# Performance work log

Hardware: AMD Instinct MI355X
Metric: run time of the kernel (lower is better)

## Reference

```python
import jax, jax.numpy as jnp
import numpy as np

N, E = 50000, 800000          # nodes, edges (before self loops)
IN_DIM, HID = 128, 96
HEADS, LAYERS = 2, 2
C = HID // HEADS              # per-head channels = 48
NEG_SLOPE = 0.2               # PyG GATv2 leaky_relu slope
EPS = 1e-5                    # LayerNorm eps


def setup_inputs() -> dict:
    key = jax.random.key(0)
    ks = jax.random.split(key, 8)
    s = 0.05
    x = jax.random.normal(ks[0], (N, IN_DIM), jnp.float32)
    edge_index = jax.random.randint(ks[1], (2, E), 0, N, jnp.int32)
    Wp = jax.random.normal(ks[2], (IN_DIM, HID), jnp.float32) * s
    bp = jnp.zeros((HID,), jnp.float32)
    g0 = jnp.ones((HID,), jnp.float32)
    b0 = jnp.zeros((HID,), jnp.float32)
    Wl = jax.random.normal(ks[3], (LAYERS, HID, HID), jnp.float32) * s
    Wr = jax.random.normal(ks[4], (LAYERS, HID, HID), jnp.float32) * s
    att = jax.random.normal(ks[5], (LAYERS, HEADS, C), jnp.float32) * s
    gs = jnp.ones((LAYERS, HID), jnp.float32)
    bs = jnp.zeros((LAYERS, HID), jnp.float32)
    return dict(x=x, edge_index=edge_index, Wp=Wp, bp=bp, g0=g0, b0=b0,
                Wl=Wl, Wr=Wr, att=att, gs=gs, bs=bs)


def layer_norm(h, g, b):
    mu = jnp.mean(h, axis=-1, keepdims=True)
    var = jnp.mean(jnp.square(h - mu), axis=-1, keepdims=True)
    return (h - mu) * jax.lax.rsqrt(var + EPS) * g + b


def gatv2_layer(h, src, dst, Wl, Wr, att):
    # GATv2Conv, bias=False, concat=True, eval-mode (no attention dropout)
    xl = (h @ Wl).reshape(N, HEADS, C)   # source transform
    xr = (h @ Wr).reshape(N, HEADS, C)   # target transform
    e = jax.nn.leaky_relu(xl[src] + xr[dst], NEG_SLOPE)   # [Et,H,C]
    score = jnp.einsum('ehc,hc->eh', e, att)              # [Et,H]
    # segment softmax over edges grouped by target node
    m = jax.ops.segment_max(score, dst, num_segments=N)   # [N,H]
    p = jnp.exp(score - m[dst])
    denom = jax.ops.segment_sum(p, dst, num_segments=N)
    alpha = p / denom[dst]                                # [Et,H]
    out = jax.ops.segment_sum(alpha[:, :, None] * xl[src], dst, num_segments=N)
    return out.reshape(N, HID)


def reference(x, edge_index, Wp, bp, g0, b0, Wl, Wr, att, gs, bs):
    # add_self_loops=True: every node gets a self edge, so every segment is non-empty
    loops = jnp.arange(N, dtype=edge_index.dtype)
    src = jnp.concatenate([edge_index[0], loops])
    dst = jnp.concatenate([edge_index[1], loops])
    # input proj -> LayerNorm -> ReLU (dropout = identity in eval)
    h = jax.nn.relu(layer_norm(x @ Wp + bp, g0, b0))
    for i in range(LAYERS):
        hn = gatv2_layer(h, src, dst, Wl[i], Wr[i], att[i])
        hn = jax.nn.elu(layer_norm(hn, gs[i], bs[i]))
        h = h + hn   # shapes always match (HID -> HID), so residual always taken
    return h
```

## Files before the change

### kernel.cpp

```cpp
#include <hip/hip_runtime.h>
#include <hip/hip_bf16.h>

#define N_NODES 50000
#define E_EDGES 800000
#define ET (E_EDGES + N_NODES)
#define IN_DIM 128
#define HID 96
#define HEADS 2
#define CPH 48
#define NEG_SLOPE 0.2f
#define LN_EPS 1e-5f
#define CHUNK 24
#define LROW 50
#define PBASE (CHUNK * LROW)
#define WTILE (PBASE + 2 * CHUNK)
#define FBLK 2048
#define WPTOT (IN_DIM * HID)
#define WCTOT (HID * 2 * HID)

typedef __hip_bfloat16 bf16;
typedef short bf16x8 __attribute__((ext_vector_type(8)));
typedef float f32x4 __attribute__((ext_vector_type(4)));
typedef _Float16 h16;
typedef h16 h16x2 __attribute__((ext_vector_type(2)));
typedef h16 h16x8 __attribute__((ext_vector_type(8)));
typedef unsigned short ushort_t;

#if __has_builtin(__builtin_amdgcn_fdot2)
#define HAS_FDOT2 1
#else
#define HAS_FDOT2 0
#endif

#define CVTPK(dst, a, b) asm("v_cvt_pk_bf16_f32 %0, %1, %2" : "=v"(dst) : "v"(a), "v"(b))

__device__ __forceinline__ unsigned short f2bf(float f) {
    union { float f; unsigned int i; } u; u.f = f;
    unsigned int r = u.i + 0x7FFFu + ((u.i >> 16) & 1u);
    return (unsigned short)(r >> 16);
}

template<int CTRL>
__device__ __forceinline__ float dpp_add(float v) {
    int m = __builtin_amdgcn_update_dpp(0, __builtin_bit_cast(int, v), CTRL, 0xf, 0xf, false);
    return v + __builtin_bit_cast(float, m);
}
__device__ __forceinline__ float half_sum(float v) {
    v = dpp_add<0x111>(v); v = dpp_add<0x112>(v); v = dpp_add<0x114>(v);
    v = dpp_add<0x118>(v); v = dpp_add<0x142>(v);
    return v;
}
__device__ __forceinline__ float wave_sum(float v) {
    v = half_sum(v); v = dpp_add<0x143>(v);
    return v;
}
__device__ __forceinline__ float rlane(float v, int lane) {
    return __builtin_bit_cast(float, __builtin_amdgcn_readlane(__builtin_bit_cast(int, v), lane));
}

__global__ void k_hist(const int* __restrict__ ei, int* __restrict__ deg) {
    int e = blockIdx.x * blockDim.x + threadIdx.x;
    if (e >= ET) return;
    int dst = (e < E_EDGES) ? ei[E_EDGES + e] : (e - E_EDGES);
    atomicAdd(&deg[dst], 1);
}

__global__ __launch_bounds__(1024) void k_scan(const int* __restrict__ deg,
                                               int* __restrict__ rowstart,
                                               int* __restrict__ cursor) {
    __shared__ int wsum[16];
    __shared__ int s_carry;
    int t = threadIdx.x, lane = t & 63, w = t >> 6;
    if (t == 0) s_carry = 0;
    __syncthreads();
    for (int base = 0; base < N_NODES; base += 4096) {
        int i0 = base + t * 4;
        int4 d = {0, 0, 0, 0};
        if (i0 + 3 < N_NODES) d = *(const int4*)(deg + i0);
        else {
            if (i0 + 0 < N_NODES) d.x = deg[i0 + 0];
            if (i0 + 1 < N_NODES) d.y = deg[i0 + 1];
            if (i0 + 2 < N_NODES) d.z = deg[i0 + 2];
            if (i0 + 3 < N_NODES) d.w = deg[i0 + 3];
        }
        int e1 = d.x, e2 = d.x + d.y, e3 = d.x + d.y + d.z;
        int tot = e3 + d.w;
        int sv = tot;
        for (int o = 1; o < 64; o <<= 1) { int u = __shfl_up(sv, o, 64); if (lane >= o) sv += u; }
        if (lane == 63) wsum[w] = sv;
        __syncthreads();
        if (w == 0) {
            int val = (lane < 16) ? wsum[lane] : 0;
            int s2 = val;
            for (int o = 1; o < 64; o <<= 1) { int u = __shfl_up(s2, o, 64); if (lane >= o) s2 += u; }
            if (lane < 16) wsum[lane] = s2 - val;
        }
        __syncthreads();
        int excl = s_carry + wsum[w] + (sv - tot);
        if (i0 + 3 < N_NODES) {
            int4 r = {excl, excl + e1, excl + e2, excl + e3};
            *(int4*)(rowstart + i0) = r;
            *(int4*)(cursor + i0) = r;
        } else {
            if (i0 + 0 < N_NODES) { rowstart[i0 + 0] = excl;      cursor[i0 + 0] = excl; }
            if (i0 + 1 < N_NODES) { rowstart[i0 + 1] = excl + e1; cursor[i0 + 1] = excl + e1; }
            if (i0 + 2 < N_NODES) { rowstart[i0 + 2] = excl + e2; cursor[i0 + 2] = excl + e2; }
            if (i0 + 3 < N_NODES) { rowstart[i0 + 3] = excl + e3; cursor[i0 + 3] = excl + e3; }
        }
        __syncthreads();
        if (t == 1023) s_carry += wsum[15] + sv;
        __syncthreads();
    }
    if (t == 0) rowstart[N_NODES] = ET;
}

__global__ void k_scatter(const int* __restrict__ ei, int* __restrict__ cursor,
                          int* __restrict__ csr_src) {
    int e = blockIdx.x * blockDim.x + threadIdx.x;
    if (e >= ET) return;
    int src, dst;
    if (e < E_EDGES) { src = ei[e]; dst = ei[E_EDGES + e]; }
    else             { src = dst = e - E_EDGES; }
    int pos = atomicAdd(&cursor[dst], 1);
    csr_src[pos] = src;
}

__global__ void k_wprep_all(const float* __restrict__ Wp,
                            const float* __restrict__ Wl,
                            const float* __restrict__ Wr,
                            unsigned short* __restrict__ wp_frag,
                            unsigned short* __restrict__ wc_frag,
                            int* __restrict__ deg) {
    int idx = blockIdx.x * blockDim.x + threadIdx.x;
    if (idx < N_NODES) deg[idx] = 0;
    if (idx < WPTOT) {
        int j = idx & 7, lane = (idx >> 3) & 63;
        int nt = (idx >> 9) % 6, ks = (idx >> 9) / 6;
        int k = ks * 32 + ((lane >> 4) << 3) + j;
        int col = nt * 16 + (lane & 15);
        wp_frag[idx] = f2bf(Wp[k * HID + col]);
    } else if (idx < WPTOT + 2 * WCTOT) {
        int L = (idx - WPTOT) / WCTOT;
        int id = (idx - WPTOT) % WCTOT;
        int j = id & 7, lane = (id >> 3) & 63;
        int nt = (id >> 9) % 12, ks = (id >> 9) / 12;
        int k = ks * 32 + ((lane >> 4) << 3) + j;
        int col = nt * 16 + (lane & 15);
        const float* W0 = Wl + (size_t)L * HID * HID;
        const float* W1 = Wr + (size_t)L * HID * HID;
        float v = (col < HID) ? W0[k * HID + col] : W1[k * HID + col - HID];
        wc_frag[(size_t)L * WCTOT + id] = f2bf(v);
    }
}

template<int K, int NT, bool PROJ>
__global__ __launch_bounds__(256) void k_gemm(const float* __restrict__ A,
                                              const ushort_t* __restrict__ Abf,
                                              const unsigned short* __restrict__ Bfrag,
                                              const float* __restrict__ bp,
                                              const float* __restrict__ g0,
                                              const float* __restrict__ b0,
                                              float* __restrict__ hout,
                                              ushort_t* __restrict__ hbout,
                                              h16* __restrict__ xl,
                                              h16* __restrict__ xr) {
    constexpr int KS = K / 32;
    constexpr int NF = KS * NT;
    __shared__ unsigned short Blds[NF * 512];
    int t = threadIdx.x, l = t & 63, w = t >> 6;
    #pragma unroll
    for (int i = 0; i < NF / 4; i++)
        ((float4*)Blds)[i * 256 + t] = ((const float4*)Bfrag)[i * 256 + t];
    __syncthreads();

    int row0 = blockIdx.x * 64 + w * 16;
    int arow = row0 + (l & 15);
    if (arow > N_NODES - 1) arow = N_NODES - 1;
    int kb = (l >> 4) * 8;
    bf16x8 a[KS];
    if constexpr (PROJ) {
        const float* ap = A + (long)arow * K + kb;
        #pragma unroll
        for (int ks = 0; ks < KS; ks++) {
            float4 f0 = *(const float4*)(ap + ks * 32);
            float4 f1 = *(const float4*)(ap + ks * 32 + 4);
            union { unsigned int u[4]; bf16x8 v; } cv;
            CVTPK(cv.u[0], f0.x, f0.y); CVTPK(cv.u[1], f0.z, f0.w);
            CVTPK(cv.u[2], f1.x, f1.y); CVTPK(cv.u[3], f1.z, f1.w);
            a[ks] = cv.v;
        }
    } else {
        const ushort_t* ap = Abf + (long)arow * K + kb;
        #pragma unroll
        for (int ks = 0; ks < KS; ks++)
            a[ks] = *(const bf16x8*)(ap + ks * 32);
    }
    f32x4 acc[NT];
    #pragma unroll
    for (int nt = 0; nt < NT; nt++) acc[nt] = (f32x4){0.f, 0.f, 0.f, 0.f};
    #pragma unroll
    for (int nt = 0; nt < NT; nt++) {
        #pragma unroll
        for (int ks = 0; ks < KS; ks++) {
            bf16x8 b = *(const bf16x8*)(Blds + (((ks * NT + nt) * 64 + l) << 3));
            acc[nt] = __builtin_amdgcn_mfma_f32_16x16x32_bf16(a[ks], b, acc[nt], 0, 0, 0);
        }
    }
    int rg = l >> 4, cl = l & 15;
    if constexpr (PROJ) {
        float bpv[NT], g0v[NT], b0v[NT];
        #pragma unroll
        for (int nt = 0; nt < NT; nt++) {
            int col = nt * 16 + cl;
            bpv[nt] = bp[col]; g0v[nt] = g0[col]; b0v[nt] = b0[col];
        }
        #pragma unroll
        for (int r = 0; r < 4; r++) {
            float s = 0.f, sq = 0.f;
            #pragma unroll
            for (int nt = 0; nt < NT; nt++) {
                float v = acc[nt][r] + bpv[nt];
                acc[nt][r] = v; s += v; sq += v * v;
            }
            #pragma unroll
            for (int o = 1; o <= 8; o <<= 1) { s += __shfl_xor(s, o, 64); sq += __shfl_xor(sq, o, 64); }
            float mu = s / (float)HID;
            float var = sq / (float)HID - mu * mu;
            float rstd = rsqrtf(var + LN_EPS);
            int row = row0 + rg * 4 + r;
            if (row < N_NODES) {
                #pragma unroll
                for (int nt = 0; nt < NT; nt++) {
                    int col = nt * 16 + cl;
                    float y = fmaxf((acc[nt][r] - mu) * rstd * g0v[nt] + b0v[nt], 0.f);
                    hout[(long)row * HID + col] = y;
                    hbout[(long)row * HID + col] = f2bf(y);
                }
            }
        }
    } else {
        #pragma unroll
        for (int r = 0; r < 4; r++) {
            int row = row0 + rg * 4 + r;
            if (row < N_NODES) {
                #pragma unroll
                for (int nt = 0; nt < NT; nt++) {
                    int col = nt * 16 + cl;
                    h16 v = (h16)acc[nt][r];
                    if (col < HID) xl[(long)row * HID + col] = v;
                    else           xr[(long)row * HID + col - HID] = v;
                }
            }
        }
    }
}

__global__ __launch_bounds__(256) void k_node_fused(const int* __restrict__ rowstart,
                                                    const int* __restrict__ csr_src,
                                                    const h16* __restrict__ xl,
                                                    const h16* __restrict__ xr,
                                                    const float* __restrict__ att,
                                                    const float* __restrict__ gs,
                                                    const float* __restrict__ bs,
                                                    float* __restrict__ h,
                                                    ushort_t* __restrict__ hb,
                                                    float* __restrict__ out,
                                                    int write_out) {
    __shared__ float lds[4 * WTILE];
    int t = threadIdx.x, lane = t & 63, w = t >> 6;
    float* slds = lds + w * WTILE;
    float* pbuf = slds + PBASE;
    int j = lane & 31, hh = lane >> 5;
    bool jok = (j < CHUNK);
    int l = lane;
    int lc = (l < 48) ? l : 47;
    bool hi = (lc >= 24);
    bool act = (l < 48);

    const float* ar = att + hh * CPH;
    h16x8 attv[6];
    #pragma unroll
    for (int v = 0; v < 6; v++) {
        float4 t0 = *(const float4*)(ar + v * 8);
        float4 t1 = *(const float4*)(ar + v * 8 + 4);
        attv[v] = (h16x8){(h16)t0.x, (h16)t0.y, (h16)t0.z, (h16)t0.w,
                          (h16)t1.x, (h16)t1.y, (h16)t1.z, (h16)t1.w};
    }

    for (int n = blockIdx.x * 4 + w; n < N_NODES; n += FBLK * 4) {
        int rs = rowstart[n], re = rowstart[n + 1];
        const h16x8* xrr = (const h16x8*)(xr + (long)n * HID + hh * CPH);
        h16x8 xrv[6];
        #pragma unroll
        for (int v = 0; v < 6; v++) xrv[v] = xrr[v];

        float Dl = 0.f;
        float2 acc = {0.f, 0.f};

        for (int base = rs; base < re; base += CHUNK) {
            int L = min(CHUNK, re - base);
            if (jok) {
                float p = 0.f;
                int srcj = csr_src[base + min(j, L - 1)];
                const h16x8* xlr = (const h16x8*)(xl + (long)srcj * HID + hh * CPH);
                float s0 = 0.f, s1 = 0.f;
#if !HAS_FDOT2
                h16x8 sacc = (h16x8)(h16)0.f;
#endif
                #pragma unroll
                for (int v = 0; v < 6; v++) {
                    h16x8 xa = xlr[v];
                    *(h16x8*)(slds + j * LROW + hh * 24 + v * 4) = xa;
                    h16x8 sum = xa + xrv[v];
                    h16x8 lk = __builtin_elementwise_max(sum, sum * (h16)NEG_SLOPE);
#if HAS_FDOT2
                    s0 = __builtin_amdgcn_fdot2(__builtin_shufflevector(lk, lk, 0, 1),
                                                __builtin_shufflevector(attv[v], attv[v], 0, 1), s0, false);
                    s1 = __builtin_amdgcn_fdot2(__builtin_shufflevector(lk, lk, 2, 3),
                                                __builtin_shufflevector(attv[v], attv[v], 2, 3), s1, false);
                    s0 = __builtin_amdgcn_fdot2(__builtin_shufflevector(lk, lk, 4, 5),
                                                __builtin_shufflevector(attv[v], attv[v], 4, 5), s0, false);
                    s1 = __builtin_amdgcn_fdot2(__builtin_shufflevector(lk, lk, 6, 7),
                                                __builtin_shufflevector(attv[v], attv[v], 6, 7), s1, false);
#else
                    sacc += lk * attv[v];
#endif
                }
#if !HAS_FDOT2
                {
                    h16x2 p0 = __builtin_shufflevector(sacc, sacc, 0, 1);
                    h16x2 p1 = __builtin_shufflevector(sacc, sacc, 2, 3);
                    h16x2 p2 = __builtin_shufflevector(sacc, sacc, 4, 5);
                    h16x2 p3 = __builtin_shufflevector(sacc, sacc, 6, 7);
                    h16x2 q = (p0 + p1) + (p2 + p3);
                    s0 = (float)q.x + (float)q.y; s1 = 0.f;
                }
#endif
                if (j < L) { p = __expf(s0 + s1); Dl += p; }
                pbuf[hh * CHUNK + j] = p;
            }
            const float* prow = pbuf + (hi ? CHUNK : 0);
            #pragma unroll
            for (int i4 = 0; i4 < CHUNK / 4; i4++) {
                if (i4 * 4 >= L) break;
                float4 pv = *(const float4*)(prow + i4 * 4);
                #pragma unroll
                for (int k = 0; k < 4; k++) {
                    h16x2 hv = ((const h16x2*)(slds + (i4 * 4 + k) * LROW))[lc];
                    float pk = ((const float*)&pv)[k];
                    acc.x += pk * (float)hv.x;
                    acc.y += pk * (float)hv.y;
                }
            }
        }
        float sh = half_sum(Dl);
        float D0 = rlane(sh, 31), D1 = rlane(sh, 63);
        float myD = hi ? D1 : D0;
        float oa = acc.x / myD, ob = acc.y / myD;
        float oaz = act ? oa : 0.f, obz = act ? ob : 0.f;
        float s1r = wave_sum(oaz + obz);
        float s2r = wave_sum(oaz * oaz + obz * obz);
        float mu = rlane(s1r, 63) / (float)HID;
        float var = rlane(s2r, 63) / (float)HID - mu * mu;
        float rstd = rsqrtf(var + LN_EPS);
        if (act) {
            long baseo = (long)n * HID + 2 * l;
            float2 g = *(const float2*)(gs + 2 * l);
            float2 b = *(const float2*)(bs + 2 * l);
            float y0 = (oaz - mu) * rstd * g.x + b.x;
            float y1 = (obz - mu) * rstd * g.y + b.y;
            float hn0 = (y0 > 0.f) ? y0 : expm1f(y0);
            float hn1 = (y1 > 0.f) ? y1 : expm1f(y1);
            float2 hold = *(float2*)(h + baseo);
            float2 hv = {hold.x + hn0, hold.y + hn1};
            *(float2*)(h + baseo) = hv;
            if (write_out) {
                *(float2*)(out + baseo) = hv;
            } else {
                unsigned int hp;
                CVTPK(hp, hv.x, hv.y);
                *(unsigned int*)(hb + baseo) = hp;
            }
        }
    }
}

extern "C" void kernel_launch(void* const* d_in, const int* in_sizes, int n_in,
                              void* d_out, int out_size, void* d_ws, size_t ws_size,
                              hipStream_t stream) {
    const float* x   = (const float*)d_in[0];
    const int*   ei  = (const int*)d_in[1];
    const float* Wp  = (const float*)d_in[2];
    const float* bp  = (const float*)d_in[3];
    const float* g0  = (const float*)d_in[4];
    const float* b0  = (const float*)d_in[5];
    const float* Wl  = (const float*)d_in[6];
    const float* Wr  = (const float*)d_in[7];
    const float* att = (const float*)d_in[8];
    const float* gs  = (const float*)d_in[9];
    const float* bs  = (const float*)d_in[10];
    float* out = (float*)d_out;

    char* wsp = (char*)d_ws;
    size_t off = 0;
    auto alloc = [&](size_t bytes) { void* p = wsp + off; off += (bytes + 255) / 256 * 256; return p; };
    float*    h       = (float*)   alloc((size_t)N_NODES * HID * 4);
    ushort_t* hb      = (ushort_t*)alloc((size_t)N_NODES * HID * 2);
    h16*      xl      = (h16*)     alloc((size_t)N_NODES * HID * 2);
    h16*      xr      = (h16*)     alloc((size_t)N_NODES * HID * 2);
    int*      deg     = (int*)     alloc((size_t)N_NODES * 4);
    int*      rowst   = (int*)     alloc((size_t)(N_NODES + 1) * 4);
    int*      cursor  = (int*)     alloc((size_t)N_NODES * 4);
    int*      csr_src = (int*)     alloc((size_t)ET * 4);
    unsigned short* wp_frag = (unsigned short*)alloc((size_t)WPTOT * 2);
    unsigned short* wc_frag = (unsigned short*)alloc((size_t)2 * WCTOT * 2);

    k_wprep_all<<<(N_NODES + 255) / 256, 256, 0, stream>>>(Wp, Wl, Wr, wp_frag, wc_frag, deg);
    k_hist<<<(ET + 255) / 256, 256, 0, stream>>>(ei, deg);
    k_scan<<<1, 1024, 0, stream>>>(deg, rowst, cursor);
    k_scatter<<<(ET + 255) / 256, 256, 0, stream>>>(ei, cursor, csr_src);

    const int GBLK = (N_NODES + 63) / 64;
    k_gemm<IN_DIM, 6, true><<<GBLK, 256, 0, stream>>>(x, nullptr, wp_frag, bp, g0, b0,
                                                      h, hb, nullptr, nullptr);
    for (int L = 0; L < 2; L++) {
        k_gemm<HID, 12, false><<<GBLK, 256, 0, stream>>>(nullptr, hb, wc_frag + (size_t)L * WCTOT,
                                                         nullptr, nullptr, nullptr,
                                                         nullptr, nullptr, xl, xr);
        k_node_fused<<<FBLK, 256, 0, stream>>>(rowst, csr_src, xl, xr,
                                               att + (size_t)L * HEADS * CPH,
                                               gs + (size_t)L * HID, bs + (size_t)L * HID,
                                               h, hb, out, (L == 1) ? 1 : 0);
    }
}
```

Baseline: 264.4 us.

## Fuse CSR scatter with input projection and prefetch next chunk of neighbor features

Merges the edge scatter kernel and the input projection GEMM into one launch, with a grid-stride scatter loop followed by the GEMM tile. This removes one launch and lets the two independent pieces of work share the device. The GEMM now loads its A operand before staging the weights into LDS, so the global loads can overlap. The node aggregation kernel software-pipelines its source-feature gathers by prefetching the next chunk's xl row into registers, which raises register pressure.

```diff
diff --git a/kernel.cpp b/kernel.cpp
--- a/kernel.cpp
+++ b/kernel.cpp
@@ -15,6 +15,7 @@
 #define PBASE (CHUNK * LROW)
 #define WTILE (PBASE + 2 * CHUNK)
 #define FBLK 2048
+#define GBLK ((N_NODES + 63) / 64)
 #define WPTOT (IN_DIM * HID)
 #define WCTOT (HID * 2 * HID)
 
@@ -112,17 +113,6 @@
         __syncthreads();
     }
     if (t == 0) rowstart[N_NODES] = ET;
-}
-
-__global__ void k_scatter(const int* __restrict__ ei, int* __restrict__ cursor,
-                          int* __restrict__ csr_src) {
-    int e = blockIdx.x * blockDim.x + threadIdx.x;
-    if (e >= ET) return;
-    int src, dst;
-    if (e < E_EDGES) { src = ei[e]; dst = ei[E_EDGES + e]; }
-    else             { src = dst = e - E_EDGES; }
-    int pos = atomicAdd(&cursor[dst], 1);
-    csr_src[pos] = src;
 }
 
 __global__ void k_wprep_all(const float* __restrict__ Wp,
@@ -154,26 +144,15 @@
 }
 
 template<int K, int NT, bool PROJ>
-__global__ __launch_bounds__(256) void k_gemm(const float* __restrict__ A,
-                                              const ushort_t* __restrict__ Abf,
-                                              const unsigned short* __restrict__ Bfrag,
-                                              const float* __restrict__ bp,
-                                              const float* __restrict__ g0,
-                                              const float* __restrict__ b0,
-                                              float* __restrict__ hout,
-                                              ushort_t* __restrict__ hbout,
-                                              h16* __restrict__ xl,
-                                              h16* __restrict__ xr) {
+__device__ __forceinline__ void gemm_tile(char* smem,
+        const float* A, const ushort_t* Abf, const ushort_t* Bfrag,
+        const float* bp, const float* g0, const float* b0,
+        float* hout, ushort_t* hbout, h16* xl, h16* xr, int bid, int t) {
     constexpr int KS = K / 32;
     constexpr int NF = KS * NT;
-    __shared__ unsigned short Blds[NF * 512];
-    int t = threadIdx.x, l = t & 63, w = t >> 6;
-    #pragma unroll
-    for (int i = 0; i < NF / 4; i++)
-        ((float4*)Blds)[i * 256 + t] = ((const float4*)Bfrag)[i * 256 + t];
-    __syncthreads();
-
-    int row0 = blockIdx.x * 64 + w * 16;
+    ushort_t* Blds = (ushort_t*)smem;
+    int l = t & 63, w = t >> 6;
+    int row0 = bid * 64 + w * 16;
     int arow = row0 + (l & 15);
     if (arow > N_NODES - 1) arow = N_NODES - 1;
     int kb = (l >> 4) * 8;
@@ -192,9 +171,12 @@
     } else {
         const ushort_t* ap = Abf + (long)arow * K + kb;
         #pragma unroll
-        for (int ks = 0; ks < KS; ks++)
-            a[ks] = *(const bf16x8*)(ap + ks * 32);
-    }
+        for (int ks = 0; ks < KS; ks++) a[ks] = *(const bf16x8*)(ap + ks * 32);
+    }
+    #pragma unroll
+    for (int i = 0; i < NF / 4; i++)
+        ((float4*)Blds)[i * 256 + t] = ((const float4*)Bfrag)[i * 256 + t];
+    __syncthreads();
     f32x4 acc[NT];
     #pragma unroll
     for (int nt = 0; nt < NT; nt++) acc[nt] = (f32x4){0.f, 0.f, 0.f, 0.f};
@@ -253,6 +235,37 @@
             }
         }
     }
+}
+
+__global__ __launch_bounds__(256) void k_scatter_proj(const int* __restrict__ ei,
+                                                      int* __restrict__ cursor,
+                                                      int* __restrict__ csr_src,
+                                                      const float* __restrict__ x,
+                                                      const ushort_t* __restrict__ wp_frag,
+                                                      const float* __restrict__ bp,
+                                                      const float* __restrict__ g0,
+                                                      const float* __restrict__ b0,
+                                                      float* __restrict__ h,
+                                                      ushort_t* __restrict__ hb) {
+    __shared__ __align__(16) char smem[WPTOT * 2];
+    int t = threadIdx.x, bid = blockIdx.x;
+    for (int e = bid * 256 + t; e < ET; e += GBLK * 256) {
+        int src, dst;
+        if (e < E_EDGES) { src = ei[e]; dst = ei[E_EDGES + e]; }
+        else             { src = dst = e - E_EDGES; }
+        int pos = atomicAdd(&cursor[dst], 1);
+        csr_src[pos] = src;
+    }
+    gemm_tile<IN_DIM, 6, true>(smem, x, nullptr, wp_frag, bp, g0, b0,
+                               h, hb, nullptr, nullptr, bid, t);
+}
+
+__global__ __launch_bounds__(256) void k_xfm(const ushort_t* __restrict__ hb,
+                                             const ushort_t* __restrict__ wc_frag,
+                                             h16* __restrict__ xl, h16* __restrict__ xr) {
+    __shared__ __align__(16) char smem[WCTOT * 2];
+    gemm_tile<HID, 12, false>(smem, nullptr, hb, wc_frag, nullptr, nullptr, nullptr,
+                              nullptr, nullptr, xl, xr, blockIdx.x, threadIdx.x);
 }
 
 __global__ __launch_bounds__(256) void k_node_fused(const int* __restrict__ rowstart,
@@ -297,19 +310,37 @@
         float Dl = 0.f;
         float2 acc = {0.f, 0.f};
 
+        h16x8 nx[6];
+        if (jok) {
+            int L0 = min(CHUNK, re - rs);
+            int s0 = csr_src[rs + min(j, L0 - 1)];
+            const h16x8* xp = (const h16x8*)(xl + (long)s0 * HID + hh * CPH);
+            #pragma unroll
+            for (int v = 0; v < 6; v++) nx[v] = xp[v];
+        }
+
         for (int base = rs; base < re; base += CHUNK) {
             int L = min(CHUNK, re - base);
             if (jok) {
+                h16x8 cc[6];
+                #pragma unroll
+                for (int v = 0; v < 6; v++) cc[v] = nx[v];
+                int nb = base + CHUNK;
+                if (nb < re) {
+                    int Ln = min(CHUNK, re - nb);
+                    int sn = csr_src[nb + min(j, Ln - 1)];
+                    const h16x8* xp = (const h16x8*)(xl + (long)sn * HID + hh * CPH);
+                    #pragma unroll
+                    for (int v = 0; v < 6; v++) nx[v] = xp[v];
+                }
                 float p = 0.f;
-                int srcj = csr_src[base + min(j, L - 1)];
-                const h16x8* xlr = (const h16x8*)(xl + (long)srcj * HID + hh * CPH);
                 float s0 = 0.f, s1 = 0.f;
 #if !HAS_FDOT2
                 h16x8 sacc = (h16x8)(h16)0.f;
 #endif
                 #pragma unroll
                 for (int v = 0; v < 6; v++) {
-                    h16x8 xa = xlr[v];
+                    h16x8 xa = cc[v];
                     *(h16x8*)(slds + j * LROW + hh * 24 + v * 4) = xa;
                     h16x8 sum = xa + xrv[v];
                     h16x8 lk = __builtin_elementwise_max(sum, sum * (h16)NEG_SLOPE);
@@ -412,21 +443,15 @@
     int*      rowst   = (int*)     alloc((size_t)(N_NODES + 1) * 4);
     int*      cursor  = (int*)     alloc((size_t)N_NODES * 4);
     int*      csr_src = (int*)     alloc((size_t)ET * 4);
-    unsigned short* wp_frag = (unsigned short*)alloc((size_t)WPTOT * 2);
-    unsigned short* wc_frag = (unsigned short*)alloc((size_t)2 * WCTOT * 2);
+    ushort_t* wp_frag = (ushort_t*)alloc((size_t)WPTOT * 2);
+    ushort_t* wc_frag = (ushort_t*)alloc((size_t)2 * WCTOT * 2);
 
     k_wprep_all<<<(N_NODES + 255) / 256, 256, 0, stream>>>(Wp, Wl, Wr, wp_frag, wc_frag, deg);
     k_hist<<<(ET + 255) / 256, 256, 0, stream>>>(ei, deg);
     k_scan<<<1, 1024, 0, stream>>>(deg, rowst, cursor);
-    k_scatter<<<(ET + 255) / 256, 256, 0, stream>>>(ei, cursor, csr_src);
-
-    const int GBLK = (N_NODES + 63) / 64;
-    k_gemm<IN_DIM, 6, true><<<GBLK, 256, 0, stream>>>(x, nullptr, wp_frag, bp, g0, b0,
-                                                      h, hb, nullptr, nullptr);
+    k_scatter_proj<<<GBLK, 256, 0, stream>>>(ei, cursor, csr_src, x, wp_frag, bp, g0, b0, h, hb);
     for (int L = 0; L < 2; L++) {
-        k_gemm<HID, 12, false><<<GBLK, 256, 0, stream>>>(nullptr, hb, wc_frag + (size_t)L * WCTOT,
-                                                         nullptr, nullptr, nullptr,
-                                                         nullptr, nullptr, xl, xr);
+        k_xfm<<<GBLK, 256, 0, stream>>>(hb, wc_frag + (size_t)L * WCTOT, xl, xr);
         k_node_fused<<<FBLK, 256, 0, stream>>>(rowst, csr_src, xl, xr,
                                                att + (size_t)L * HEADS * CPH,
                                                gs + (size_t)L * HID, bs + (size_t)L * HID,
```

Result: slower. 336.4 us (+27.2%).
